# Optimization experiments

Measured on AMD Instinct MI355X. Metric: run time of the kernel, lower is better.

The kernel has to match this reference:

```python
import jax, jax.numpy as jnp
import numpy as np

L_ITERS = 8   # number of ReduNet layers
C = 10        # number of classes
D = 1024      # feature dimension
N = 4096      # number of samples (columns of Z)


def setup_inputs() -> dict:
    key = jax.random.key(0)
    k0, k1, k2, k3 = jax.random.split(key, 4)
    Z = jax.random.normal(k0, (D, N), dtype=jnp.float32)
    # column-normalized features, as the net maintains at every layer
    Z = Z / jnp.linalg.norm(Z, axis=0, keepdims=True)
    # Elist[l]: (D,D) expansion operator; Cslist[l]: (C,D,D) per-class compression operators
    Elist = jax.random.normal(k1, (L_ITERS, D, D), dtype=jnp.float32) / np.float32(np.sqrt(D))
    Cslist = jax.random.normal(k2, (L_ITERS, C, D, D), dtype=jnp.float32) / np.float32(np.sqrt(D))
    gamma = jax.random.uniform(k3, (C,), dtype=jnp.float32)
    gamma = gamma / jnp.sum(gamma)
    eta = jnp.asarray(0.5, dtype=jnp.float32)
    temperature = jnp.asarray(0.1, dtype=jnp.float32)
    return {"Z": Z, "Elist": Elist, "Cslist": Cslist, "gamma": gamma,
            "eta": eta, "temperature": temperature, "L": L_ITERS}


def reference(Z, Elist, Cslist, gamma, eta, temperature, L):
    for l in range(L):
        Cs = Cslist[l]                                   # (C, d, d)
        CZ = jnp.einsum('cij,jn->cin', Cs, Z)            # (C, d, n)
        sims = -jnp.sqrt(jnp.sum(CZ * CZ, axis=1))       # fro norm over dim=1 -> (C, n)
        P_hat = jax.nn.softmax(sims / temperature, axis=0)  # softmax over classes
        PZ = P_hat[:, None, :] * Z                       # (C, d, n)
        term = jnp.einsum('c,cij,cjn->in', gamma, Cs, PZ)   # gamma-weighted class compression
        grads = Elist[l] @ Z - term                      # (d, n)
        Z = Z + eta * grads
        Z = Z / jnp.linalg.norm(Z, axis=0, keepdims=True)   # column-wise normalization
    return Z
```

## Files before the change

kernel.cpp:

```cpp
#include <hip/hip_runtime.h>
#include <hip/hip_bf16.h>
#include <stdint.h>

#define D_DIM 1024
#define N_DIM 4096
#define C_CLS 10
#define L_IT 8
#define M_DIM 11264
#define NBM 44

typedef __bf16 bf16_t;
typedef __bf16 bf16x8 __attribute__((ext_vector_type(8)));
typedef __bf16 bf16x4 __attribute__((ext_vector_type(4)));
typedef float  f32x4  __attribute__((ext_vector_type(4)));

__device__ __forceinline__ float bf2f(uint16_t u) {
  union { uint32_t i; float f; } x; x.i = ((uint32_t)u) << 16; return x.f;
}

__global__ void pack_bf16_k(const float4* __restrict__ src, bf16x4* __restrict__ dst, int n4) {
  int stride = gridDim.x * blockDim.x;
  for (int i = blockIdx.x * blockDim.x + threadIdx.x; i < n4; i += stride) {
    float4 v = src[i];
    bf16x4 o;
    o[0] = (bf16_t)v.x; o[1] = (bf16_t)v.y; o[2] = (bf16_t)v.z; o[3] = (bf16_t)v.w;
    dst[i] = o;
  }
}

__global__ __launch_bounds__(256) void transpose_zbt(const float* __restrict__ Zsrc,
                                                     bf16_t* __restrict__ ZbT,
                                                     float* __restrict__ Zf_copy,
                                                     const float* __restrict__ normsq) {
  __shared__ float tile[32][33];
  int tx = threadIdx.x & 31, ty = threadIdx.x >> 5;
  int nb = blockIdx.x, db = blockIdx.y;
  int n = nb * 32 + tx;
  float inv = normsq ? rsqrtf(normsq[n]) : 1.0f;
#pragma unroll
  for (int j = 0; j < 32; j += 8) {
    int d = db * 32 + ty + j;
    float v = Zsrc[(size_t)d * N_DIM + n];
    if (Zf_copy) Zf_copy[(size_t)d * N_DIM + n] = v;
    tile[ty + j][tx] = v * inv;
  }
  __syncthreads();
  int d2 = db * 32 + tx;
#pragma unroll
  for (int j = 0; j < 32; j += 8) {
    int n2 = nb * 32 + ty + j;
    ZbT[(size_t)n2 * D_DIM + d2] = (bf16_t)tile[tx][ty + j];
  }
}


#define STAGE_A(buf, h, t) do {                                                         \
    _Pragma("unroll") for (int e_ = 0; e_ < 2; ++e_) {                                  \
      const bf16_t* s_ = Wb + aoff0[e_] + (size_t)(h) * 65536 + (size_t)(t) * 64;       \
      __builtin_amdgcn_global_load_lds(                                                 \
        (const __attribute__((address_space(1))) void*)s_,                              \
        (__attribute__((address_space(3))) void*)(lds + (buf)*16384 + (h)*8192 + dstslot[e_]), \
        16, 0, 0);                                                                      \
    } } while (0)

#define STAGE_B(buf, h, t) do {                                                         \
    _Pragma("unroll") for (int e_ = 0; e_ < 2; ++e_) {                                  \
      const bf16_t* s_ = ZbT + boff0[e_] + (size_t)(h) * 32768 + (size_t)(t) * 64;      \
      __builtin_amdgcn_global_load_lds(                                                 \
        (const __attribute__((address_space(1))) void*)s_,                              \
        (__attribute__((address_space(3))) void*)(lds + 32768 + (buf)*16384 + (h)*8192 + dstslot[e_]), \
        16, 0, 0);                                                                      \
    } } while (0)

#define LOAD_A(buf, qm) do {                                                            \
    _Pragma("unroll") for (int f_ = 0; f_ < 4; ++f_)                                    \
      _Pragma("unroll") for (int kk_ = 0; kk_ < 2; ++kk_)                               \
        a[f_][kk_] = *(const bf16x8*)(lds + (buf)*16384 + (qm)*8192 + aRowBase + f_*1024 + sidx[kk_]); \
  } while (0)

#define LOAD_B(buf, qn) do {                                                            \
    _Pragma("unroll") for (int f_ = 0; f_ < 2; ++f_)                                    \
      _Pragma("unroll") for (int kk_ = 0; kk_ < 2; ++kk_)                               \
        b[f_][kk_] = *(const bf16x8*)(lds + 32768 + (buf)*16384 + (qn)*8192 + bRowBase + f_*1024 + sidx[kk_]); \
  } while (0)

#define MFMA_Q(qm, qn) do {                                                             \
    _Pragma("unroll") for (int mm_ = 0; mm_ < 4; ++mm_)                                 \
      _Pragma("unroll") for (int nn_ = 0; nn_ < 2; ++nn_)                               \
        _Pragma("unroll") for (int kk_ = 0; kk_ < 2; ++kk_)                             \
          acc[(qm)*4+mm_][(qn)*2+nn_] = __builtin_amdgcn_mfma_f32_16x16x32_bf16(        \
            a[mm_][kk_], b[nn_][kk_], acc[(qm)*4+mm_][(qn)*2+nn_], 0, 0, 0);            \
  } while (0)

#define PHASE(buf, qm, qn, DO_LOADA, STAGE_STMT, WAIT_STMT) do {                        \
    if (DO_LOADA) LOAD_A(buf, qm);                                                      \
    LOAD_B(buf, qn);                                                                    \
    STAGE_STMT;                                                                         \
    __builtin_amdgcn_s_barrier();                                                       \
    asm volatile("s_waitcnt lgkmcnt(0)" ::: "memory");                                  \
    __builtin_amdgcn_sched_barrier(0);                                                  \
    __builtin_amdgcn_s_setprio(1);                                                      \
    MFMA_Q(qm, qn);                                                                     \
    __builtin_amdgcn_s_setprio(0);                                                      \
    WAIT_STMT;                                                                          \
    __builtin_amdgcn_s_barrier();                                                       \
  } while (0)

__global__ __launch_bounds__(512, 2) void gemm_wz8(const bf16_t* __restrict__ Wb,
                                                   const bf16_t* __restrict__ ZbT,
                                                   bf16_t* __restrict__ OUT, int ldo,
                                                   float* __restrict__ ssq) {
  __shared__ __align__(16) bf16_t lds[65536];

  int nwg = gridDim.x;
  int bid = blockIdx.x;
  int q = nwg >> 3, r = nwg & 7;
  int xcd = bid & 7, idx = bid >> 3;
  int swz = (xcd < r ? xcd * (q + 1) : r * (q + 1) + (xcd - r) * q) + idx;
  int bm = swz % NBM, bn = swz / NBM;
  int m0 = bm * 256, n0 = bn * 256;

  int tid = threadIdx.x;
  int wave = tid >> 6, lane = tid & 63;
  int wrow = wave >> 2, wcol = wave & 3;
  int lm = lane & 15, lks = lane >> 4;
  int sw = lm & 7;

  size_t aoff0[2], boff0[2];
  int dstslot[2];
#pragma unroll
  for (int e = 0; e < 2; ++e) {
    int j = e * 512 + tid;
    int rih = j >> 3, sl = j & 7;
    int sg = sl ^ (rih & 7);
    int arow = (rih & 63) + ((rih >> 6) << 7);
    int brow = (rih & 31) + ((rih >> 5) << 6);
    aoff0[e] = (size_t)(m0 + arow) * 1024 + sg * 8;
    boff0[e] = (size_t)(n0 + brow) * 1024 + sg * 8;
    dstslot[e] = e * 4096 + wave * 512;
  }

  int aRowBase = (wrow * 64 + lm) * 64;
  int bRowBase = (wcol * 32 + lm) * 64;
  int sidx[2] = { ((0 + lks) ^ sw) * 8, ((4 + lks) ^ sw) * 8 };

  f32x4 acc[8][4] = {};
  bf16x8 a[4][2], b[2][2];

  STAGE_A(0, 0, 0); STAGE_A(0, 1, 0); STAGE_B(0, 0, 0); STAGE_B(0, 1, 0);
  STAGE_A(1, 0, 1); STAGE_B(1, 0, 1);
  asm volatile("s_waitcnt vmcnt(4)" ::: "memory");
  __builtin_amdgcn_s_barrier();

  for (int it = 0; it < 7; ++it) {
    int tO = 2 * it + 1, tN = 2 * it + 2, tM = 2 * it + 3;
    PHASE(0, 0, 0, 1, STAGE_A(1, 1, tO), );
    PHASE(0, 0, 1, 0, STAGE_B(1, 1, tO), );
    PHASE(0, 1, 0, 1, STAGE_A(0, 0, tN), );
    PHASE(0, 1, 1, 0, STAGE_A(0, 1, tN), asm volatile("s_waitcnt vmcnt(4)" ::: "memory"));
    PHASE(1, 0, 0, 1, STAGE_B(0, 0, tN), );
    PHASE(1, 0, 1, 0, STAGE_B(0, 1, tN), );
    PHASE(1, 1, 0, 1, STAGE_A(1, 0, tM), );
    PHASE(1, 1, 1, 0, STAGE_B(1, 0, tM), asm volatile("s_waitcnt vmcnt(4)" ::: "memory"));
  }
  PHASE(0, 0, 0, 1, STAGE_A(1, 1, 15), );
  PHASE(0, 0, 1, 0, STAGE_B(1, 1, 15), );
  PHASE(0, 1, 0, 1, , );
  PHASE(0, 1, 1, 0, , asm volatile("s_waitcnt vmcnt(0)" ::: "memory"));
  PHASE(1, 0, 0, 1, , );
  PHASE(1, 0, 1, 0, , );
  PHASE(1, 1, 0, 1, , );
  PHASE(1, 1, 1, 0, , );

  int orow = (lane >> 4) * 4;
#pragma unroll
  for (int mf = 0; mf < 8; ++mf)
#pragma unroll
    for (int nf = 0; nf < 4; ++nf) {
      int col = n0 + wcol * 64 + nf * 16 + lm;
      size_t rb = (size_t)(m0 + wrow * 128 + mf * 16 + orow) * ldo + col;
#pragma unroll
      for (int rr = 0; rr < 4; ++rr)
        OUT[rb + (size_t)rr * ldo] = (bf16_t)acc[mf][nf][rr];
    }

  if (m0 < C_CLS * 1024) {
    int c = m0 >> 10;
#pragma unroll
    for (int nf = 0; nf < 4; ++nf) {
      float v = 0.f;
#pragma unroll
      for (int mf = 0; mf < 8; ++mf)
#pragma unroll
        for (int rr = 0; rr < 4; ++rr)
          v += acc[mf][nf][rr] * acc[mf][nf][rr];
      v += __shfl_xor(v, 16);
      v += __shfl_xor(v, 32);
      if (lks == 0)
        atomicAdd(&ssq[(size_t)c * ldo + n0 + wcol * 64 + nf * 16 + lm], v);
    }
  }
}

__global__ __launch_bounds__(256) void update_fused(const bf16_t* __restrict__ OUT, int ldo, int Nc,
                                                    const float* __restrict__ ssq,
                                                    const float* __restrict__ gamma,
                                                    const float* __restrict__ etap,
                                                    const float* __restrict__ tempr,
                                                    const float* __restrict__ normsq_old,
                                                    float* __restrict__ Zf, int n_off,
                                                    float* __restrict__ normsq_new) {
  int nl = blockIdx.x * 256 + threadIdx.x;
  if (nl >= Nc) return;
  int n = n_off + nl;
  int i0 = blockIdx.y * 64;
  float eta = etap[0], invT = 1.0f / tempr[0];
  float zs = normsq_old ? rsqrtf(normsq_old[n]) : 1.0f;

  float s[C_CLS], m = -1e30f;
#pragma unroll
  for (int c = 0; c < C_CLS; ++c) {
    float sim = -sqrtf(ssq[(size_t)c * ldo + nl]);
    s[c] = sim;
    m = fmaxf(m, sim);
  }
  float sum = 0.f;
#pragma unroll
  for (int c = 0; c < C_CLS; ++c) {
    float e = __expf((s[c] - m) * invT);
    s[c] = e;
    sum += e;
  }
  float invsum = 1.0f / sum;
  float gP[C_CLS];
#pragma unroll
  for (int c = 0; c < C_CLS; ++c) gP[c] = gamma[c] * s[c] * invsum;

  const uint16_t* ob = (const uint16_t*)OUT + nl;
  float ss = 0.f;
  for (int i = i0; i < i0 + 64; ++i) {
    float term = 0.f;
#pragma unroll
    for (int c = 0; c < C_CLS; ++c)
      term += gP[c] * bf2f(ob[(size_t)((c << 10) + i) * ldo]);
    float g = bf2f(ob[(size_t)(10240 + i) * ldo]);
    float z = Zf[(size_t)i * N_DIM + n] * zs;
    float zn = z + eta * (g - term);
    Zf[(size_t)i * N_DIM + n] = zn;
    ss += zn * zn;
  }
  atomicAdd(&normsq_new[n], ss);
}

__global__ void normalize_z(float* __restrict__ Zf, const float* __restrict__ normsq) {
  int n = blockIdx.x * 256 + threadIdx.x;
  int i = blockIdx.y;
  float inv = rsqrtf(normsq[n]);
  Zf[(size_t)i * N_DIM + n] *= inv;
}

extern "C" void kernel_launch(void* const* d_in, const int* in_sizes, int n_in,
                              void* d_out, int out_size, void* d_ws, size_t ws_size,
                              hipStream_t stream) {
  (void)in_sizes; (void)n_in; (void)out_size;
  const float* Zin        = (const float*)d_in[0];
  const float* Elist      = (const float*)d_in[1];
  const float* Cslist     = (const float*)d_in[2];
  const float* gamma      = (const float*)d_in[3];
  const float* eta        = (const float*)d_in[4];
  const float* temperature= (const float*)d_in[5];

  float* Zf = (float*)d_out;

  auto align256 = [](size_t x) { return (x + 255) & ~(size_t)255; };
  size_t zbt_b = align256((size_t)N_DIM * D_DIM * 2);
  size_t wb_b  = align256((size_t)M_DIM * D_DIM * 2);
  size_t ns_b  = align256((size_t)N_DIM * 4);
  size_t fixed = zbt_b + wb_b + 2 * ns_b;

  int Nc = N_DIM;
  while (Nc > 256) {
    size_t need = fixed + align256((size_t)C_CLS * Nc * 4) + align256((size_t)M_DIM * Nc * 2);
    if (need <= ws_size) break;
    Nc >>= 1;
  }
  if (fixed + align256((size_t)C_CLS * Nc * 4) + align256((size_t)M_DIM * Nc * 2) > ws_size) {
    hipMemsetAsync(d_out, 0, (size_t)D_DIM * N_DIM * 4, stream);
    return;
  }

  char* p = (char*)d_ws;
  bf16_t* ZbT  = (bf16_t*)p; p += zbt_b;
  bf16_t* Wb   = (bf16_t*)p; p += wb_b;
  float*  nsA  = (float*)p;  p += ns_b;
  float*  nsB  = (float*)p;  p += ns_b;
  float*  ssq  = (float*)p;  p += align256((size_t)C_CLS * Nc * 4);
  bf16_t* OUT  = (bf16_t*)p;

  float* ns_cur = nullptr;
  for (int l = 0; l < L_IT; ++l) {
    const float* Cs = Cslist + (size_t)l * C_CLS * D_DIM * D_DIM;
    const float* El = Elist  + (size_t)l * D_DIM * D_DIM;
    pack_bf16_k<<<2048, 256, 0, stream>>>((const float4*)Cs, (bf16x4*)Wb,
                                          C_CLS * D_DIM * D_DIM / 4);
    pack_bf16_k<<<1024, 256, 0, stream>>>((const float4*)El,
                                          (bf16x4*)(Wb + (size_t)C_CLS * D_DIM * D_DIM),
                                          D_DIM * D_DIM / 4);
    transpose_zbt<<<dim3(N_DIM / 32, D_DIM / 32), 256, 0, stream>>>(
        l == 0 ? Zin : Zf, ZbT, l == 0 ? Zf : nullptr, ns_cur);

    float* ns_new = (ns_cur == nsA) ? nsB : nsA;
    hipMemsetAsync(ns_new, 0, (size_t)N_DIM * 4, stream);

    for (int n_off = 0; n_off < N_DIM; n_off += Nc) {
      hipMemsetAsync(ssq, 0, (size_t)C_CLS * Nc * 4, stream);
      gemm_wz8<<<dim3(NBM * (Nc / 256)), 512, 0, stream>>>(
          Wb, ZbT + (size_t)n_off * D_DIM, OUT, Nc, ssq);
      update_fused<<<dim3((Nc + 255) / 256, D_DIM / 64), 256, 0, stream>>>(
          OUT, Nc, Nc, ssq, gamma, eta, temperature, ns_cur, Zf, n_off, ns_new);
    }
    ns_cur = ns_new;
  }
  normalize_z<<<dim3(N_DIM / 256, D_DIM), 256, 0, stream>>>(Zf, ns_cur);
}
```

Measured before the change: 1.314 ms.

## Keep Z transposed across layers and fuse column normalization into update

Z is now kept in a transposed fp32 buffer plus a bf16 copy, both written directly by a new per-column update kernel. The GEMM output is also stored transposed. Each wave handles one column: it reduces that column's norm with shuffles, normalizes it, and writes both the fp32 and bf16 copies. This removes the per-layer transpose kernel, the norm memset, the atomic norm accumulation and the separate normalize pass, leaving only one transpose at the start and one at the end. The cost is an extra fp32 workspace buffer and GEMM output stores that are strided by the M dimension.

```diff
diff --git a/kernel.cpp b/kernel.cpp
--- a/kernel.cpp
+++ b/kernel.cpp
@@ -13,6 +13,7 @@
 typedef __bf16 bf16x8 __attribute__((ext_vector_type(8)));
 typedef __bf16 bf16x4 __attribute__((ext_vector_type(4)));
 typedef float  f32x4  __attribute__((ext_vector_type(4)));
+typedef unsigned short u16x8 __attribute__((ext_vector_type(8)));
 
 __device__ __forceinline__ float bf2f(uint16_t u) {
   union { uint32_t i; float f; } x; x.i = ((uint32_t)u) << 16; return x.f;
@@ -28,28 +29,46 @@
   }
 }
 
-__global__ __launch_bounds__(256) void transpose_zbt(const float* __restrict__ Zsrc,
-                                                     bf16_t* __restrict__ ZbT,
-                                                     float* __restrict__ Zf_copy,
-                                                     const float* __restrict__ normsq) {
+__global__ __launch_bounds__(256) void init_zt(const float* __restrict__ Zin,
+                                               float* __restrict__ ZfT,
+                                               bf16_t* __restrict__ ZbT) {
   __shared__ float tile[32][33];
   int tx = threadIdx.x & 31, ty = threadIdx.x >> 5;
   int nb = blockIdx.x, db = blockIdx.y;
   int n = nb * 32 + tx;
-  float inv = normsq ? rsqrtf(normsq[n]) : 1.0f;
 #pragma unroll
   for (int j = 0; j < 32; j += 8) {
     int d = db * 32 + ty + j;
-    float v = Zsrc[(size_t)d * N_DIM + n];
-    if (Zf_copy) Zf_copy[(size_t)d * N_DIM + n] = v;
-    tile[ty + j][tx] = v * inv;
+    tile[ty + j][tx] = Zin[(size_t)d * N_DIM + n];
   }
   __syncthreads();
   int d2 = db * 32 + tx;
 #pragma unroll
   for (int j = 0; j < 32; j += 8) {
     int n2 = nb * 32 + ty + j;
-    ZbT[(size_t)n2 * D_DIM + d2] = (bf16_t)tile[tx][ty + j];
+    float v = tile[tx][ty + j];
+    ZfT[(size_t)n2 * D_DIM + d2] = v;
+    ZbT[(size_t)n2 * D_DIM + d2] = (bf16_t)v;
+  }
+}
+
+__global__ __launch_bounds__(256) void final_out(const float* __restrict__ ZfT,
+                                                 float* __restrict__ outp) {
+  __shared__ float tile[32][33];
+  int tx = threadIdx.x & 31, ty = threadIdx.x >> 5;
+  int nb = blockIdx.x, db = blockIdx.y;
+#pragma unroll
+  for (int j = 0; j < 32; j += 8) {
+    int n = nb * 32 + ty + j;
+    int d = db * 32 + tx;
+    tile[ty + j][tx] = ZfT[(size_t)n * D_DIM + d];
+  }
+  __syncthreads();
+#pragma unroll
+  for (int j = 0; j < 32; j += 8) {
+    int d2 = db * 32 + ty + j;
+    int n2 = nb * 32 + tx;
+    outp[(size_t)d2 * N_DIM + n2] = tile[tx][ty + j];
   }
 }
 
@@ -108,7 +127,7 @@
 
 __global__ __launch_bounds__(512, 2) void gemm_wz8(const bf16_t* __restrict__ Wb,
                                                    const bf16_t* __restrict__ ZbT,
-                                                   bf16_t* __restrict__ OUT, int ldo,
+                                                   bf16_t* __restrict__ OUT_T, int ldn,
                                                    float* __restrict__ ssq) {
   __shared__ __align__(16) bf16_t lds[65536];
 
@@ -172,16 +191,16 @@
   PHASE(1, 1, 0, 1, , );
   PHASE(1, 1, 1, 0, , );
 
-  int orow = (lane >> 4) * 4;
 #pragma unroll
   for (int mf = 0; mf < 8; ++mf)
 #pragma unroll
     for (int nf = 0; nf < 4; ++nf) {
       int col = n0 + wcol * 64 + nf * 16 + lm;
-      size_t rb = (size_t)(m0 + wrow * 128 + mf * 16 + orow) * ldo + col;
-#pragma unroll
-      for (int rr = 0; rr < 4; ++rr)
-        OUT[rb + (size_t)rr * ldo] = (bf16_t)acc[mf][nf][rr];
+      int row = m0 + wrow * 128 + mf * 16 + lks * 4;
+      bf16x4 v;
+#pragma unroll
+      for (int rr = 0; rr < 4; ++rr) v[rr] = (bf16_t)acc[mf][nf][rr];
+      *(bf16x4*)(OUT_T + (size_t)col * M_DIM + row) = v;
     }
 
   if (m0 < C_CLS * 1024) {
@@ -197,30 +216,29 @@
       v += __shfl_xor(v, 16);
       v += __shfl_xor(v, 32);
       if (lks == 0)
-        atomicAdd(&ssq[(size_t)c * ldo + n0 + wcol * 64 + nf * 16 + lm], v);
+        atomicAdd(&ssq[(size_t)c * ldn + n0 + wcol * 64 + nf * 16 + lm], v);
     }
   }
 }
 
-__global__ __launch_bounds__(256) void update_fused(const bf16_t* __restrict__ OUT, int ldo, int Nc,
-                                                    const float* __restrict__ ssq,
-                                                    const float* __restrict__ gamma,
-                                                    const float* __restrict__ etap,
-                                                    const float* __restrict__ tempr,
-                                                    const float* __restrict__ normsq_old,
-                                                    float* __restrict__ Zf, int n_off,
-                                                    float* __restrict__ normsq_new) {
-  int nl = blockIdx.x * 256 + threadIdx.x;
+__global__ __launch_bounds__(256) void update2(const bf16_t* __restrict__ OUT_T, int Nc,
+                                               const float* __restrict__ ssq,
+                                               const float* __restrict__ gamma,
+                                               const float* __restrict__ etap,
+                                               const float* __restrict__ tempr,
+                                               float* __restrict__ ZfT,
+                                               bf16_t* __restrict__ ZbT,
+                                               int n_off) {
+  int wv = threadIdx.x >> 6, lane = threadIdx.x & 63;
+  int nl = blockIdx.x * 4 + wv;
   if (nl >= Nc) return;
   int n = n_off + nl;
-  int i0 = blockIdx.y * 64;
   float eta = etap[0], invT = 1.0f / tempr[0];
-  float zs = normsq_old ? rsqrtf(normsq_old[n]) : 1.0f;
 
   float s[C_CLS], m = -1e30f;
 #pragma unroll
   for (int c = 0; c < C_CLS; ++c) {
-    float sim = -sqrtf(ssq[(size_t)c * ldo + nl]);
+    float sim = -sqrtf(ssq[(size_t)c * Nc + nl]);
     s[c] = sim;
     m = fmaxf(m, sim);
   }
@@ -236,27 +254,51 @@
 #pragma unroll
   for (int c = 0; c < C_CLS; ++c) gP[c] = gamma[c] * s[c] * invsum;
 
-  const uint16_t* ob = (const uint16_t*)OUT + nl;
+  const u16x8* ob = (const u16x8*)(OUT_T + (size_t)nl * M_DIM) + lane * 2;
+  float term[16] = {};
+#pragma unroll
+  for (int c = 0; c < C_CLS; ++c) {
+    u16x8 v0 = ob[c * 128], v1 = ob[c * 128 + 1];
+#pragma unroll
+    for (int j = 0; j < 8; ++j) {
+      term[j]     += gP[c] * bf2f(v0[j]);
+      term[8 + j] += gP[c] * bf2f(v1[j]);
+    }
+  }
+  u16x8 g0 = ob[C_CLS * 128], g1 = ob[C_CLS * 128 + 1];
+
+  const f32x4* zp = (const f32x4*)(ZfT + (size_t)n * D_DIM) + lane * 4;
+  f32x4 z[4] = { zp[0], zp[1], zp[2], zp[3] };
+
+  float zn[16];
   float ss = 0.f;
-  for (int i = i0; i < i0 + 64; ++i) {
-    float term = 0.f;
-#pragma unroll
-    for (int c = 0; c < C_CLS; ++c)
-      term += gP[c] * bf2f(ob[(size_t)((c << 10) + i) * ldo]);
-    float g = bf2f(ob[(size_t)(10240 + i) * ldo]);
-    float z = Zf[(size_t)i * N_DIM + n] * zs;
-    float zn = z + eta * (g - term);
-    Zf[(size_t)i * N_DIM + n] = zn;
-    ss += zn * zn;
-  }
-  atomicAdd(&normsq_new[n], ss);
-}
-
-__global__ void normalize_z(float* __restrict__ Zf, const float* __restrict__ normsq) {
-  int n = blockIdx.x * 256 + threadIdx.x;
-  int i = blockIdx.y;
-  float inv = rsqrtf(normsq[n]);
-  Zf[(size_t)i * N_DIM + n] *= inv;
+#pragma unroll
+  for (int j = 0; j < 16; ++j) {
+    float g = bf2f(j < 8 ? g0[j & 7] : g1[j & 7]);
+    float v = z[j >> 2][j & 3] + eta * (g - term[j]);
+    zn[j] = v;
+    ss += v * v;
+  }
+#pragma unroll
+  for (int k = 1; k < 64; k <<= 1) ss += __shfl_xor(ss, k);
+  float inv = rsqrtf(ss);
+
+  f32x4* zo = (f32x4*)(ZfT + (size_t)n * D_DIM) + lane * 4;
+  bf16x8* bo = (bf16x8*)(ZbT + (size_t)n * D_DIM) + lane * 2;
+#pragma unroll
+  for (int q4 = 0; q4 < 4; ++q4) {
+    f32x4 o;
+#pragma unroll
+    for (int j = 0; j < 4; ++j) o[j] = zn[q4 * 4 + j] * inv;
+    zo[q4] = o;
+  }
+#pragma unroll
+  for (int h = 0; h < 2; ++h) {
+    bf16x8 o;
+#pragma unroll
+    for (int j = 0; j < 8; ++j) o[j] = (bf16_t)(zn[h * 8 + j] * inv);
+    bo[h] = o;
+  }
 }
 
 extern "C" void kernel_launch(void* const* d_in, const int* in_sizes, int n_in,
@@ -270,13 +312,11 @@
   const float* eta        = (const float*)d_in[4];
   const float* temperature= (const float*)d_in[5];
 
-  float* Zf = (float*)d_out;
-
   auto align256 = [](size_t x) { return (x + 255) & ~(size_t)255; };
   size_t zbt_b = align256((size_t)N_DIM * D_DIM * 2);
+  size_t zft_b = align256((size_t)N_DIM * D_DIM * 4);
   size_t wb_b  = align256((size_t)M_DIM * D_DIM * 2);
-  size_t ns_b  = align256((size_t)N_DIM * 4);
-  size_t fixed = zbt_b + wb_b + 2 * ns_b;
+  size_t fixed = zbt_b + zft_b + wb_b;
 
   int Nc = N_DIM;
   while (Nc > 256) {
@@ -291,13 +331,13 @@
 
   char* p = (char*)d_ws;
   bf16_t* ZbT  = (bf16_t*)p; p += zbt_b;
+  float*  ZfT  = (float*)p;  p += zft_b;
   bf16_t* Wb   = (bf16_t*)p; p += wb_b;
-  float*  nsA  = (float*)p;  p += ns_b;
-  float*  nsB  = (float*)p;  p += ns_b;
   float*  ssq  = (float*)p;  p += align256((size_t)C_CLS * Nc * 4);
-  bf16_t* OUT  = (bf16_t*)p;
-
-  float* ns_cur = nullptr;
+  bf16_t* OUT_T= (bf16_t*)p;
+
+  init_zt<<<dim3(N_DIM / 32, D_DIM / 32), 256, 0, stream>>>(Zin, ZfT, ZbT);
+
   for (int l = 0; l < L_IT; ++l) {
     const float* Cs = Cslist + (size_t)l * C_CLS * D_DIM * D_DIM;
     const float* El = Elist  + (size_t)l * D_DIM * D_DIM;
@@ -306,20 +346,14 @@
     pack_bf16_k<<<1024, 256, 0, stream>>>((const float4*)El,
                                           (bf16x4*)(Wb + (size_t)C_CLS * D_DIM * D_DIM),
                                           D_DIM * D_DIM / 4);
-    transpose_zbt<<<dim3(N_DIM / 32, D_DIM / 32), 256, 0, stream>>>(
-        l == 0 ? Zin : Zf, ZbT, l == 0 ? Zf : nullptr, ns_cur);
-
-    float* ns_new = (ns_cur == nsA) ? nsB : nsA;
-    hipMemsetAsync(ns_new, 0, (size_t)N_DIM * 4, stream);
 
     for (int n_off = 0; n_off < N_DIM; n_off += Nc) {
       hipMemsetAsync(ssq, 0, (size_t)C_CLS * Nc * 4, stream);
       gemm_wz8<<<dim3(NBM * (Nc / 256)), 512, 0, stream>>>(
-          Wb, ZbT + (size_t)n_off * D_DIM, OUT, Nc, ssq);
-      update_fused<<<dim3((Nc + 255) / 256, D_DIM / 64), 256, 0, stream>>>(
-          OUT, Nc, Nc, ssq, gamma, eta, temperature, ns_cur, Zf, n_off, ns_new);
+          Wb, ZbT + (size_t)n_off * D_DIM, OUT_T, Nc, ssq);
+      update2<<<dim3(Nc / 4), 256, 0, stream>>>(
+          OUT_T, Nc, ssq, gamma, eta, temperature, ZfT, ZbT, n_off);
     }
-    ns_cur = ns_new;
-  }
-  normalize_z<<<dim3(N_DIM / 256, D_DIM), 256, 0, stream>>>(Zf, ns_cur);
-}
+  }
+  final_out<<<dim3(N_DIM / 32, D_DIM / 32), 256, 0, stream>>>(ZfT, (float*)d_out);
+}
```

After: 1.278 ms. 1.03x faster.
